# Kernel optimization log

Measured on AMD Instinct MI355X. Metric: run time of the kernel, lower is better.

## Reference

```python
import jax, jax.numpy as jnp
import numpy as np

N_NODES = 100000
N_EDGES = 1200000
N_DIM = 64


def setup_inputs() -> dict:
    key = jax.random.key(0)
    k1, k2, k3 = jax.random.split(key, 3)
    all_emb = jax.random.normal(k1, (N_NODES, N_DIM), dtype=jnp.float32) * 0.1
    edge_vals = jax.random.uniform(k2, (N_EDGES,), dtype=jnp.float32)
    edge_index = jax.random.randint(k3, (2, N_EDGES), 0, N_NODES, dtype=jnp.int64)
    return {"all_emb": all_emb, "edge_vals": edge_vals, "edge_index": edge_index, "n_layers": 3}


def _spmm(edge_vals, edge_index, x):
    # sparse.mm: out[dst] += val * x[src]; edge_index[0]=row(dst), edge_index[1]=col(src)
    dst, src = edge_index[0], edge_index[1]
    msgs = edge_vals[:, None] * x[src]          # [E, D] gather + scale
    return jax.ops.segment_sum(msgs, dst, num_segments=x.shape[0])


def reference(all_emb, edge_vals, edge_index, n_layers):
    # Fused layer-mean accumulation (avoids stacking all intermediates).
    emb = all_emb
    acc = all_emb
    for _ in range(n_layers):
        emb = _spmm(edge_vals, edge_index, emb)
        acc = acc + emb
    return acc / jnp.float32(n_layers + 1)
```

## Files before the change

### kernel.cpp

```cpp
#include <hip/hip_runtime.h>
#include <hip/hip_bf16.h>
#include <hip/hip_fp16.h>

#define D 64
#define P2_GRID 256
#define KITER 19
#define CHUNK (KITER*256)
#define KMAX 512
#define CAP 4096
#define SCAP 4608
#define CASTB 392

__device__ __forceinline__ unsigned f32_to_bf16_rne(float f) {
    unsigned u = __float_as_uint(f);
    return (u + 0x7FFFu + ((u >> 16) & 1u)) >> 16;
}
__device__ __forceinline__ float bfu(unsigned short w) {
    return __uint_as_float((unsigned)w << 16);
}
__device__ __forceinline__ float hv(unsigned s) {
    return __half2float(__ushort_as_half((unsigned short)(s >> 17)));
}

__global__ __launch_bounds__(256) void p2_bin_cast(const int* __restrict__ ei,
                                                   const float* __restrict__ vals,
                                                   int* __restrict__ gcur,
                                                   unsigned long long* __restrict__ region,
                                                   const float4* __restrict__ emb4,
                                                   uint2* __restrict__ x0,
                                                   int n4, int E, int K) {
    __shared__ unsigned long long stage[CHUNK];
    __shared__ int hist[KMAX], sstart[KMAX], sbase[KMAX];
    __shared__ int wsum[4], woff[4];

    if (blockIdx.x >= P2_GRID) {
        int i0 = (blockIdx.x - P2_GRID) * 256 + threadIdx.x;
        for (int i = i0; i < n4; i += CASTB * 256) {
            float4 v = emb4[i];
            uint2 o;
            o.x = f32_to_bf16_rne(v.x) | (f32_to_bf16_rne(v.y) << 16);
            o.y = f32_to_bf16_rne(v.z) | (f32_to_bf16_rne(v.w) << 16);
            x0[i] = o;
        }
        return;
    }

    int t  = threadIdx.x;
    int c0 = blockIdx.x * CHUNK;
    int cnt = E - c0; if (cnt > CHUNK) cnt = CHUNK; if (cnt < 0) cnt = 0;

    hist[t] = 0; hist[t + 256] = 0;
    __syncthreads();

    unsigned long long ent[KITER];
    int rk[KITER];
    #pragma unroll
    for (int k = 0; k < KITER; ++k) {
        int i = t + k * 256;
        rk[k] = -1;
        if (i < cnt) {
            int e   = c0 + i;
            int dst = ei[e];
            int src = ei[E + e];
            unsigned h16 = (unsigned)__half_as_ushort(__float2half(vals[e]));
            int b = dst >> 8;
            ent[k] = ((unsigned long long)b << 41)
                   | ((unsigned long long)h16 << 25)
                   | ((unsigned long long)(dst & 0xFF) << 17)
                   | (unsigned long long)src;
            rk[k] = atomicAdd(&hist[b], 1);
        }
    }
    __syncthreads();

    int h0 = hist[2 * t], h1 = hist[2 * t + 1];
    int p  = h0 + h1;
    int lane = t & 63, w = t >> 6;
    int x = p;
    #pragma unroll
    for (int off = 1; off < 64; off <<= 1) {
        int y = __shfl_up(x, off, 64);
        if (lane >= off) x += y;
    }
    if (lane == 63) wsum[w] = x;
    __syncthreads();
    if (t < 4) {
        int e = 0;
        for (int i = 0; i < t; ++i) e += wsum[i];
        woff[t] = e;
    }
    __syncthreads();
    int excl = x - p + woff[w];
    sstart[2 * t]     = excl;
    sstart[2 * t + 1] = excl + h0;
    __syncthreads();

    for (int b = t; b < K; b += 256)
        sbase[b] = hist[b] ? atomicAdd(&gcur[b], hist[b]) : 0;

    #pragma unroll
    for (int k = 0; k < KITER; ++k) {
        if (rk[k] >= 0)
            stage[sstart[(int)(ent[k] >> 41)] + rk[k]] = ent[k];
    }
    __syncthreads();

    for (int i = t; i < cnt; i += 256) {
        unsigned long long e = stage[i];
        int b = (int)(e >> 41);
        int gidx = sbase[b] + (i - sstart[b]);
        if (gidx < CAP)
            region[((size_t)b << 12) | gidx] = e;
    }
}

__global__ __launch_bounds__(256) void p3_csr(const unsigned long long* __restrict__ region,
                                              const int* __restrict__ gcur,
                                              unsigned* __restrict__ gslots,
                                              unsigned* __restrict__ rowinfo,
                                              int N) {
    __shared__ unsigned outstage[SCAP];
    __shared__ int rcnt[256], rstart[256];
    __shared__ int wsum[4], woff[4];
    __shared__ int stot;
    int b = blockIdx.x, t = threadIdx.x;
    int cnt = gcur[b]; if (cnt > CAP) cnt = CAP;
    const unsigned long long* reg = region + ((size_t)b << 12);

    rcnt[t] = 0;
    __syncthreads();

    unsigned long long ent[16];
    int rk[16];
    #pragma unroll
    for (int k = 0; k < 16; ++k) {
        int i = t + k * 256;
        rk[k] = -1;
        if (i < cnt) {
            ent[k] = reg[i];
            rk[k]  = atomicAdd(&rcnt[(int)(ent[k] >> 17) & 0xFF], 1);
        }
    }
    __syncthreads();

    int rc  = rcnt[t]; if (rc > 56) rc = 56;
    int rcp = (rc + 7) & ~7;
    int lane = t & 63, w = t >> 6;
    int x = rcp;
    #pragma unroll
    for (int off = 1; off < 64; off <<= 1) {
        int y = __shfl_up(x, off, 64);
        if (lane >= off) x += y;
    }
    if (lane == 63) wsum[w] = x;
    __syncthreads();
    if (t < 4) {
        int e = 0;
        for (int i = 0; i < t; ++i) e += wsum[i];
        woff[t] = e;
    }
    __syncthreads();
    int rs = x - rcp + woff[w];
    rstart[t] = rs;
    if (t == 255) stot = rs + rcp;
    __syncthreads();

    #pragma unroll
    for (int k = 0; k < 16; ++k) {
        if (rk[k] >= 0 && rk[k] < 56) {
            int pos = rstart[(int)(ent[k] >> 17) & 0xFF] + rk[k];
            if (pos < SCAP)
                outstage[pos] = ((unsigned)((ent[k] >> 25) & 0x7FFF) << 17)
                              | (unsigned)(ent[k] & 0x1FFFF);
        }
    }
    for (int i = rs + rc; i < rs + rcp; ++i)
        if (i >= 0 && i < SCAP) outstage[i] = 0u;
    __syncthreads();

    int ptot = stot; if (ptot > SCAP) ptot = SCAP;
    size_t gb = (size_t)b * SCAP;
    for (int i = t; i < ptot; i += 256)
        gslots[gb + i] = outstage[i];
    int row = (b << 8) | t;
    if (row < N) {
        int ni = rcp >> 3;
        if (rs >= SCAP) ni = 0;
        else if (rs + (ni << 3) > SCAP) ni = (SCAP - rs) >> 3;
        rowinfo[row] = ((unsigned)(gb + (size_t)rs) << 4) | (unsigned)ni;
    }
}

__global__ __launch_bounds__(256) void spmm8(const unsigned short* __restrict__ xs,
                                             const unsigned* __restrict__ gslots,
                                             const unsigned* __restrict__ rowinfo,
                                             unsigned short* __restrict__ nexts,
                                             const unsigned short* __restrict__ x0s,
                                             const unsigned short* __restrict__ h1s,
                                             float* __restrict__ outf,
                                             int mode, int N) {
    int gid = blockIdx.x * blockDim.x + threadIdx.x;
    int row = __builtin_amdgcn_readfirstlane(gid >> 6);
    if (row >= N) return;
    int lane = gid & 63;
    unsigned info = rowinfo[row];
    int niter = (int)(info & 15u);
    const unsigned* s = gslots + (info >> 4);

    float sum = 0.f;
    for (int it = 0; it < niter; ++it, s += 8) {
        unsigned s0 = s[0], s1 = s[1], s2 = s[2], s3 = s[3],
                 s4 = s[4], s5 = s[5], s6 = s[6], s7 = s[7];
        unsigned short w0 = xs[((size_t)(s0 & 0x1FFFFu) << 6) | lane];
        unsigned short w1 = xs[((size_t)(s1 & 0x1FFFFu) << 6) | lane];
        unsigned short w2 = xs[((size_t)(s2 & 0x1FFFFu) << 6) | lane];
        unsigned short w3 = xs[((size_t)(s3 & 0x1FFFFu) << 6) | lane];
        unsigned short w4 = xs[((size_t)(s4 & 0x1FFFFu) << 6) | lane];
        unsigned short w5 = xs[((size_t)(s5 & 0x1FFFFu) << 6) | lane];
        unsigned short w6 = xs[((size_t)(s6 & 0x1FFFFu) << 6) | lane];
        unsigned short w7 = xs[((size_t)(s7 & 0x1FFFFu) << 6) | lane];
        sum += hv(s0) * bfu(w0);
        sum += hv(s1) * bfu(w1);
        sum += hv(s2) * bfu(w2);
        sum += hv(s3) * bfu(w3);
        sum += hv(s4) * bfu(w4);
        sum += hv(s5) * bfu(w5);
        sum += hv(s6) * bfu(w6);
        sum += hv(s7) * bfu(w7);
    }

    int o = (row << 6) | lane;
    if (mode != 2) {
        nexts[o] = (unsigned short)f32_to_bf16_rne(sum);
    } else {
        outf[o] = (bfu(x0s[o]) + bfu(h1s[o]) + bfu(xs[o]) + sum) * 0.25f;
    }
}

extern "C" void kernel_launch(void* const* d_in, const int* in_sizes, int n_in,
                              void* d_out, int out_size, void* d_ws, size_t ws_size,
                              hipStream_t stream) {
    const float* all_emb   = (const float*)d_in[0];
    const float* edge_vals = (const float*)d_in[1];
    const int*   edge_idx  = (const int*)d_in[2];

    const int E = in_sizes[1];
    const int n = out_size;
    const int N = n / D;
    const int K = (N + 255) >> 8;
    float* out = (float*)d_out;

    unsigned long long* region = (unsigned long long*)d_ws;
    unsigned* gslots  = (unsigned*)(region + (size_t)K * CAP);
    unsigned* rowinfo = gslots + (size_t)K * SCAP;
    int*      gcur    = (int*)(rowinfo + N);
    unsigned* X0      = (unsigned*)(gcur + ((K + 1) & ~1));
    unsigned* X1      = X0 + n / 2;
    unsigned* X2      = X1 + n / 2;

    const int TB = 256;
    const int grid_spmm = (N * 64 + TB - 1) / TB;

    hipMemsetAsync(gcur, 0, (size_t)K * sizeof(int), stream);
    p2_bin_cast<<<P2_GRID + CASTB, TB, 0, stream>>>(edge_idx, edge_vals, gcur, region,
                                                    (const float4*)all_emb, (uint2*)X0,
                                                    n / 4, E, K);
    p3_csr<<<K, TB, 0, stream>>>(region, gcur, gslots, rowinfo, N);

    spmm8<<<grid_spmm, TB, 0, stream>>>((const unsigned short*)X0, gslots, rowinfo,
                                        (unsigned short*)X1, nullptr, nullptr, nullptr, 0, N);
    spmm8<<<grid_spmm, TB, 0, stream>>>((const unsigned short*)X1, gslots, rowinfo,
                                        (unsigned short*)X2, nullptr, nullptr, nullptr, 1, N);
    spmm8<<<grid_spmm, TB, 0, stream>>>((const unsigned short*)X2, gslots, rowinfo,
                                        nullptr, (const unsigned short*)X0,
                                        (const unsigned short*)X1, out, 2, N);
}
```

Measured before the change: 232.6 us.

## Merge build and SpMM stages into two cooperative kernels with grid syncs

Replaces the memset, binning, CSR-build and three SpMM launches with two cooperative kernels that use grid-wide syncs between phases. The build kernel zeroes counters, bins edges and casts embeddings, then builds the CSR slots. The SpMM kernel runs all three layers over a persistent grid of 1024 blocks with grid-stride rows. This removes launch gaps and the memset, but adds grid-sync cost, limits occupancy to co-resident blocks, and makes the shared-memory union large (about 40KB).

```diff
diff --git a/kernel.cpp b/kernel.cpp
--- a/kernel.cpp
+++ b/kernel.cpp
@@ -1,6 +1,9 @@
 #include <hip/hip_runtime.h>
+#include <hip/hip_cooperative_groups.h>
 #include <hip/hip_bf16.h>
 #include <hip/hip_fp16.h>
+
+namespace cg = cooperative_groups;
 
 #define D 64
 #define P2_GRID 256
@@ -10,6 +13,8 @@
 #define CAP 4096
 #define SCAP 4608
 #define CASTB 392
+#define BGRID (P2_GRID + CASTB)
+#define SGRID 1024
 
 __device__ __forceinline__ unsigned f32_to_bf16_rne(float f) {
     unsigned u = __float_as_uint(f);
@@ -22,19 +27,37 @@
     return __half2float(__ushort_as_half((unsigned short)(s >> 17)));
 }
 
-__global__ __launch_bounds__(256) void p2_bin_cast(const int* __restrict__ ei,
-                                                   const float* __restrict__ vals,
-                                                   int* __restrict__ gcur,
-                                                   unsigned long long* __restrict__ region,
-                                                   const float4* __restrict__ emb4,
-                                                   uint2* __restrict__ x0,
-                                                   int n4, int E, int K) {
-    __shared__ unsigned long long stage[CHUNK];
-    __shared__ int hist[KMAX], sstart[KMAX], sbase[KMAX];
-    __shared__ int wsum[4], woff[4];
+struct P2S {
+    unsigned long long stage[CHUNK];
+    int hist[KMAX], sstart[KMAX], sbase[KMAX];
+    int wsum[4], woff[4];
+};
+struct P3S {
+    unsigned outstage[SCAP];
+    int rcnt[256], rstart[256];
+    int wsum[4], woff[4], stot;
+};
+union SHU { P2S p2; P3S p3; };
+
+__global__ __launch_bounds__(256) void build_all(const int* __restrict__ ei,
+                                                 const float* __restrict__ vals,
+                                                 int* __restrict__ gcur,
+                                                 unsigned long long* __restrict__ region,
+                                                 unsigned* __restrict__ gslots,
+                                                 unsigned* __restrict__ rowinfo,
+                                                 const float4* __restrict__ emb4,
+                                                 uint2* __restrict__ x0,
+                                                 int n4, int E, int N, int K) {
+    __shared__ SHU sh;
+    cg::grid_group grid = cg::this_grid();
+    int t = threadIdx.x;
+
+    int gi = blockIdx.x * 256 + t;
+    if (gi < K) gcur[gi] = 0;
+    grid.sync();
 
     if (blockIdx.x >= P2_GRID) {
-        int i0 = (blockIdx.x - P2_GRID) * 256 + threadIdx.x;
+        int i0 = (blockIdx.x - P2_GRID) * 256 + t;
         for (int i = i0; i < n4; i += CASTB * 256) {
             float4 v = emb4[i];
             uint2 o;
@@ -42,92 +65,82 @@
             o.y = f32_to_bf16_rne(v.z) | (f32_to_bf16_rne(v.w) << 16);
             x0[i] = o;
         }
-        return;
-    }
-
-    int t  = threadIdx.x;
-    int c0 = blockIdx.x * CHUNK;
-    int cnt = E - c0; if (cnt > CHUNK) cnt = CHUNK; if (cnt < 0) cnt = 0;
-
-    hist[t] = 0; hist[t + 256] = 0;
-    __syncthreads();
-
-    unsigned long long ent[KITER];
-    int rk[KITER];
-    #pragma unroll
-    for (int k = 0; k < KITER; ++k) {
-        int i = t + k * 256;
-        rk[k] = -1;
-        if (i < cnt) {
-            int e   = c0 + i;
-            int dst = ei[e];
-            int src = ei[E + e];
-            unsigned h16 = (unsigned)__half_as_ushort(__float2half(vals[e]));
-            int b = dst >> 8;
-            ent[k] = ((unsigned long long)b << 41)
-                   | ((unsigned long long)h16 << 25)
-                   | ((unsigned long long)(dst & 0xFF) << 17)
-                   | (unsigned long long)src;
-            rk[k] = atomicAdd(&hist[b], 1);
-        }
-    }
-    __syncthreads();
-
-    int h0 = hist[2 * t], h1 = hist[2 * t + 1];
-    int p  = h0 + h1;
-    int lane = t & 63, w = t >> 6;
-    int x = p;
-    #pragma unroll
-    for (int off = 1; off < 64; off <<= 1) {
-        int y = __shfl_up(x, off, 64);
-        if (lane >= off) x += y;
-    }
-    if (lane == 63) wsum[w] = x;
-    __syncthreads();
-    if (t < 4) {
-        int e = 0;
-        for (int i = 0; i < t; ++i) e += wsum[i];
-        woff[t] = e;
-    }
-    __syncthreads();
-    int excl = x - p + woff[w];
-    sstart[2 * t]     = excl;
-    sstart[2 * t + 1] = excl + h0;
-    __syncthreads();
-
-    for (int b = t; b < K; b += 256)
-        sbase[b] = hist[b] ? atomicAdd(&gcur[b], hist[b]) : 0;
-
-    #pragma unroll
-    for (int k = 0; k < KITER; ++k) {
-        if (rk[k] >= 0)
-            stage[sstart[(int)(ent[k] >> 41)] + rk[k]] = ent[k];
-    }
-    __syncthreads();
-
-    for (int i = t; i < cnt; i += 256) {
-        unsigned long long e = stage[i];
-        int b = (int)(e >> 41);
-        int gidx = sbase[b] + (i - sstart[b]);
-        if (gidx < CAP)
-            region[((size_t)b << 12) | gidx] = e;
-    }
-}
-
-__global__ __launch_bounds__(256) void p3_csr(const unsigned long long* __restrict__ region,
-                                              const int* __restrict__ gcur,
-                                              unsigned* __restrict__ gslots,
-                                              unsigned* __restrict__ rowinfo,
-                                              int N) {
-    __shared__ unsigned outstage[SCAP];
-    __shared__ int rcnt[256], rstart[256];
-    __shared__ int wsum[4], woff[4];
-    __shared__ int stot;
-    int b = blockIdx.x, t = threadIdx.x;
+    } else {
+        int c0 = blockIdx.x * CHUNK;
+        int cnt = E - c0; if (cnt > CHUNK) cnt = CHUNK; if (cnt < 0) cnt = 0;
+
+        sh.p2.hist[t] = 0; sh.p2.hist[t + 256] = 0;
+        __syncthreads();
+
+        unsigned long long ent[KITER];
+        int rk[KITER];
+        #pragma unroll
+        for (int k = 0; k < KITER; ++k) {
+            int i = t + k * 256;
+            rk[k] = -1;
+            if (i < cnt) {
+                int e   = c0 + i;
+                int dst = ei[e];
+                int src = ei[E + e];
+                unsigned h16 = (unsigned)__half_as_ushort(__float2half(vals[e]));
+                int b = dst >> 8;
+                ent[k] = ((unsigned long long)b << 41)
+                       | ((unsigned long long)h16 << 25)
+                       | ((unsigned long long)(dst & 0xFF) << 17)
+                       | (unsigned long long)src;
+                rk[k] = atomicAdd(&sh.p2.hist[b], 1);
+            }
+        }
+        __syncthreads();
+
+        int h0 = sh.p2.hist[2 * t], h1 = sh.p2.hist[2 * t + 1];
+        int p  = h0 + h1;
+        int lane = t & 63, w = t >> 6;
+        int x = p;
+        #pragma unroll
+        for (int off = 1; off < 64; off <<= 1) {
+            int y = __shfl_up(x, off, 64);
+            if (lane >= off) x += y;
+        }
+        if (lane == 63) sh.p2.wsum[w] = x;
+        __syncthreads();
+        if (t < 4) {
+            int e = 0;
+            for (int i = 0; i < t; ++i) e += sh.p2.wsum[i];
+            sh.p2.woff[t] = e;
+        }
+        __syncthreads();
+        int excl = x - p + sh.p2.woff[w];
+        sh.p2.sstart[2 * t]     = excl;
+        sh.p2.sstart[2 * t + 1] = excl + h0;
+        __syncthreads();
+
+        for (int b = t; b < K; b += 256)
+            sh.p2.sbase[b] = sh.p2.hist[b] ? atomicAdd(&gcur[b], sh.p2.hist[b]) : 0;
+
+        #pragma unroll
+        for (int k = 0; k < KITER; ++k) {
+            if (rk[k] >= 0)
+                sh.p2.stage[sh.p2.sstart[(int)(ent[k] >> 41)] + rk[k]] = ent[k];
+        }
+        __syncthreads();
+
+        for (int i = t; i < cnt; i += 256) {
+            unsigned long long e = sh.p2.stage[i];
+            int b = (int)(e >> 41);
+            int gidx = sh.p2.sbase[b] + (i - sh.p2.sstart[b]);
+            if (gidx < CAP)
+                region[((size_t)b << 12) | gidx] = e;
+        }
+    }
+    grid.sync();
+
+    int b = blockIdx.x;
+    if (b >= K) return;
     int cnt = gcur[b]; if (cnt > CAP) cnt = CAP;
     const unsigned long long* reg = region + ((size_t)b << 12);
 
-    rcnt[t] = 0;
+    sh.p3.rcnt[t] = 0;
     __syncthreads();
 
     unsigned long long ent[16];
@@ -138,12 +151,12 @@
         rk[k] = -1;
         if (i < cnt) {
             ent[k] = reg[i];
-            rk[k]  = atomicAdd(&rcnt[(int)(ent[k] >> 17) & 0xFF], 1);
-        }
-    }
-    __syncthreads();
-
-    int rc  = rcnt[t]; if (rc > 56) rc = 56;
+            rk[k]  = atomicAdd(&sh.p3.rcnt[(int)(ent[k] >> 17) & 0xFF], 1);
+        }
+    }
+    __syncthreads();
+
+    int rc  = sh.p3.rcnt[t]; if (rc > 56) rc = 56;
     int rcp = (rc + 7) & ~7;
     int lane = t & 63, w = t >> 6;
     int x = rcp;
@@ -152,36 +165,36 @@
         int y = __shfl_up(x, off, 64);
         if (lane >= off) x += y;
     }
-    if (lane == 63) wsum[w] = x;
+    if (lane == 63) sh.p3.wsum[w] = x;
     __syncthreads();
     if (t < 4) {
         int e = 0;
-        for (int i = 0; i < t; ++i) e += wsum[i];
-        woff[t] = e;
-    }
-    __syncthreads();
-    int rs = x - rcp + woff[w];
-    rstart[t] = rs;
-    if (t == 255) stot = rs + rcp;
+        for (int i = 0; i < t; ++i) e += sh.p3.wsum[i];
+        sh.p3.woff[t] = e;
+    }
+    __syncthreads();
+    int rs = x - rcp + sh.p3.woff[w];
+    sh.p3.rstart[t] = rs;
+    if (t == 255) sh.p3.stot = rs + rcp;
     __syncthreads();
 
     #pragma unroll
     for (int k = 0; k < 16; ++k) {
         if (rk[k] >= 0 && rk[k] < 56) {
-            int pos = rstart[(int)(ent[k] >> 17) & 0xFF] + rk[k];
+            int pos = sh.p3.rstart[(int)(ent[k] >> 17) & 0xFF] + rk[k];
             if (pos < SCAP)
-                outstage[pos] = ((unsigned)((ent[k] >> 25) & 0x7FFF) << 17)
-                              | (unsigned)(ent[k] & 0x1FFFF);
+                sh.p3.outstage[pos] = ((unsigned)((ent[k] >> 25) & 0x7FFF) << 17)
+                                    | (unsigned)(ent[k] & 0x1FFFF);
         }
     }
     for (int i = rs + rc; i < rs + rcp; ++i)
-        if (i >= 0 && i < SCAP) outstage[i] = 0u;
-    __syncthreads();
-
-    int ptot = stot; if (ptot > SCAP) ptot = SCAP;
+        if (i >= 0 && i < SCAP) sh.p3.outstage[i] = 0u;
+    __syncthreads();
+
+    int ptot = sh.p3.stot; if (ptot > SCAP) ptot = SCAP;
     size_t gb = (size_t)b * SCAP;
     for (int i = t; i < ptot; i += 256)
-        gslots[gb + i] = outstage[i];
+        gslots[gb + i] = sh.p3.outstage[i];
     int row = (b << 8) | t;
     if (row < N) {
         int ni = rcp >> 3;
@@ -191,22 +204,11 @@
     }
 }
 
-__global__ __launch_bounds__(256) void spmm8(const unsigned short* __restrict__ xs,
-                                             const unsigned* __restrict__ gslots,
-                                             const unsigned* __restrict__ rowinfo,
-                                             unsigned short* __restrict__ nexts,
-                                             const unsigned short* __restrict__ x0s,
-                                             const unsigned short* __restrict__ h1s,
-                                             float* __restrict__ outf,
-                                             int mode, int N) {
-    int gid = blockIdx.x * blockDim.x + threadIdx.x;
-    int row = __builtin_amdgcn_readfirstlane(gid >> 6);
-    if (row >= N) return;
-    int lane = gid & 63;
-    unsigned info = rowinfo[row];
+__device__ __forceinline__ float row_sum(const unsigned short* __restrict__ xs,
+                                         const unsigned* __restrict__ gslots,
+                                         unsigned info, int lane) {
     int niter = (int)(info & 15u);
     const unsigned* s = gslots + (info >> 4);
-
     float sum = 0.f;
     for (int it = 0; it < niter; ++it, s += 8) {
         unsigned s0 = s[0], s1 = s[1], s2 = s[2], s3 = s[3],
@@ -228,26 +230,53 @@
         sum += hv(s6) * bfu(w6);
         sum += hv(s7) * bfu(w7);
     }
-
-    int o = (row << 6) | lane;
-    if (mode != 2) {
-        nexts[o] = (unsigned short)f32_to_bf16_rne(sum);
-    } else {
-        outf[o] = (bfu(x0s[o]) + bfu(h1s[o]) + bfu(xs[o]) + sum) * 0.25f;
+    return sum;
+}
+
+__global__ __launch_bounds__(256) void spmm_coop(const unsigned short* __restrict__ X0,
+                                                 unsigned short* __restrict__ X1,
+                                                 unsigned short* __restrict__ X2,
+                                                 const unsigned* __restrict__ gslots,
+                                                 const unsigned* __restrict__ rowinfo,
+                                                 float* __restrict__ outf,
+                                                 int N) {
+    cg::grid_group grid = cg::this_grid();
+    int wid  = blockIdx.x * 4 + (threadIdx.x >> 6);
+    int nw   = gridDim.x * 4;
+    int lane = threadIdx.x & 63;
+
+    for (int row = wid; row < N; row += nw) {
+        int r = __builtin_amdgcn_readfirstlane(row);
+        float sum = row_sum(X0, gslots, rowinfo[r], lane);
+        X1[(r << 6) | lane] = (unsigned short)f32_to_bf16_rne(sum);
+    }
+    grid.sync();
+    for (int row = wid; row < N; row += nw) {
+        int r = __builtin_amdgcn_readfirstlane(row);
+        float sum = row_sum(X1, gslots, rowinfo[r], lane);
+        X2[(r << 6) | lane] = (unsigned short)f32_to_bf16_rne(sum);
+    }
+    grid.sync();
+    for (int row = wid; row < N; row += nw) {
+        int r = __builtin_amdgcn_readfirstlane(row);
+        float sum = row_sum(X2, gslots, rowinfo[r], lane);
+        int o = (r << 6) | lane;
+        outf[o] = (bfu(X0[o]) + bfu(X1[o]) + bfu(X2[o]) + sum) * 0.25f;
     }
 }
 
 extern "C" void kernel_launch(void* const* d_in, const int* in_sizes, int n_in,
                               void* d_out, int out_size, void* d_ws, size_t ws_size,
                               hipStream_t stream) {
+    const int*   edge_idx  = (const int*)d_in[2];
+    const float* edge_vals = (const float*)d_in[1];
     const float* all_emb   = (const float*)d_in[0];
-    const float* edge_vals = (const float*)d_in[1];
-    const int*   edge_idx  = (const int*)d_in[2];
-
-    const int E = in_sizes[1];
-    const int n = out_size;
-    const int N = n / D;
-    const int K = (N + 255) >> 8;
+
+    int E = in_sizes[1];
+    int n = out_size;
+    int N = n / D;
+    int K = (N + 255) >> 8;
+    int n4 = n / 4;
     float* out = (float*)d_out;
 
     unsigned long long* region = (unsigned long long*)d_ws;
@@ -258,20 +287,21 @@
     unsigned* X1      = X0 + n / 2;
     unsigned* X2      = X1 + n / 2;
 
-    const int TB = 256;
-    const int grid_spmm = (N * 64 + TB - 1) / TB;
-
-    hipMemsetAsync(gcur, 0, (size_t)K * sizeof(int), stream);
-    p2_bin_cast<<<P2_GRID + CASTB, TB, 0, stream>>>(edge_idx, edge_vals, gcur, region,
-                                                    (const float4*)all_emb, (uint2*)X0,
-                                                    n / 4, E, K);
-    p3_csr<<<K, TB, 0, stream>>>(region, gcur, gslots, rowinfo, N);
-
-    spmm8<<<grid_spmm, TB, 0, stream>>>((const unsigned short*)X0, gslots, rowinfo,
-                                        (unsigned short*)X1, nullptr, nullptr, nullptr, 0, N);
-    spmm8<<<grid_spmm, TB, 0, stream>>>((const unsigned short*)X1, gslots, rowinfo,
-                                        (unsigned short*)X2, nullptr, nullptr, nullptr, 1, N);
-    spmm8<<<grid_spmm, TB, 0, stream>>>((const unsigned short*)X2, gslots, rowinfo,
-                                        nullptr, (const unsigned short*)X0,
-                                        (const unsigned short*)X1, out, 2, N);
-}
+    const float4*   emb4 = (const float4*)all_emb;
+    uint2*          x0v  = (uint2*)X0;
+    unsigned short* X0s  = (unsigned short*)X0;
+    unsigned short* X1s  = (unsigned short*)X1;
+    unsigned short* X2s  = (unsigned short*)X2;
+
+    void* bargs[] = { (void*)&edge_idx, (void*)&edge_vals, (void*)&gcur,
+                      (void*)&region, (void*)&gslots, (void*)&rowinfo,
+                      (void*)&emb4, (void*)&x0v, (void*)&n4, (void*)&E,
+                      (void*)&N, (void*)&K };
+    hipLaunchCooperativeKernel((void*)build_all, dim3(BGRID), dim3(256),
+                               bargs, 0, stream);
+
+    void* sargs[] = { (void*)&X0s, (void*)&X1s, (void*)&X2s,
+                      (void*)&gslots, (void*)&rowinfo, (void*)&out, (void*)&N };
+    hipLaunchCooperativeKernel((void*)spmm_coop, dim3(SGRID), dim3(256),
+                               sargs, 0, stream);
+}
```

Result: slower. 605.8 us (+160.4%).
